# Kernel tuning notes

Hardware: AMD Instinct MI355X
Metric: run time of the kernel (lower is better)

The kernel has to match this reference:

```python
import jax, jax.numpy as jnp
import numpy as np

N = 100000
E = 1000000
IN_C, HID, OUT_C = 64, 64, 40


def setup_inputs() -> dict:
    key = jax.random.key(0)
    ks = jax.random.split(key, 12)
    x = jax.random.normal(ks[0], (N, IN_C), dtype=jnp.float32)
    edge_index = jax.random.randint(ks[1], (2, E), 0, N, dtype=jnp.int64)

    def glorot(k, fan_in, fan_out):
        s = (6.0 / (fan_in + fan_out)) ** 0.5
        return jax.random.uniform(k, (fan_in, fan_out), jnp.float32, -s, s)

    return {
        "x": x,
        "edge_index": edge_index,
        "W1": glorot(ks[2], IN_C, HID), "b1": jnp.zeros((HID,), jnp.float32),
        "W2": glorot(ks[3], HID, HID), "b2": jnp.zeros((HID,), jnp.float32),
        "Wm1": glorot(ks[4], HID, HID), "bm1": jnp.zeros((HID,), jnp.float32),
        "Wm2": glorot(ks[5], HID, OUT_C), "bm2": jnp.zeros((OUT_C,), jnp.float32),
    }


def _gcn_conv(h_in, W, b, src, dst, deg_inv_sqrt):
    # PyG GCNConv: x' = D^{-1/2} (A + I) D^{-1/2} (x W) + b, self-loops added.
    h = h_in @ W                                        # [N, F]
    norm = deg_inv_sqrt[src] * deg_inv_sqrt[dst]        # [E]
    msg = h[src] * norm[:, None]                        # gather + scale
    agg = jax.ops.segment_sum(msg, dst, num_segments=N)  # scatter-add
    # self-loop contribution: deg_i^{-1/2} * deg_i^{-1/2} * h_i
    agg = agg + h * (deg_inv_sqrt * deg_inv_sqrt)[:, None]
    return agg + b


def reference(x, edge_index, W1, b1, W2, b2, Wm1, bm1, Wm2, bm2):
    src, dst = edge_index[0], edge_index[1]
    deg = jax.ops.segment_sum(jnp.ones((E,), jnp.float32), dst, num_segments=N) + 1.0
    deg_inv_sqrt = jax.lax.rsqrt(deg)

    h = _gcn_conv(x, W1, b1, src, dst, deg_inv_sqrt)
    h = jax.nn.relu(h)
    h = _gcn_conv(h, W2, b2, src, dst, deg_inv_sqrt)  # no relu after last conv

    h = jax.nn.relu(h @ Wm1 + bm1)
    out = h @ Wm2 + bm2
    return out
```

## Files before the change

### kernel.cpp

```cpp
#include <hip/hip_runtime.h>
#include <hip/hip_bf16.h>
#include <hip/hip_fp16.h>


namespace {

constexpr int N_NODES = 100000;
constexpr int N_EDGES = 1000000;
constexpr int NBUCK = (N_NODES + 511) / 512;
constexpr int CAP = 8192;
constexpr int EPB_A = 2048;

__global__ __launch_bounds__(256) void zero_detect_kernel(int* bucketCnt, int* flag,
                                                          const unsigned int* __restrict__ w) {
  int t = threadIdx.x;
  if (t < NBUCK) bucketCnt[t] = 0;
  if (t == 0) *flag = 0;
  __syncthreads();
  unsigned any = 0;
  for (int s = 0; s < 8; s++) {
    long long pos = ((long long)(t * 8 + s) * 104729LL) % N_EDGES;
    any |= w[2 * pos + 1];
  }
  if (any) atomicOr(flag, 1);
}

__global__ __launch_bounds__(256) void bucket_kernel(const void* __restrict__ ei,
                                                     const int* __restrict__ flag,
                                                     int* __restrict__ bucketCnt,
                                                     unsigned* __restrict__ tmp) {
  __shared__ int hist[NBUCK];
  __shared__ int basePB[NBUCK];
  __shared__ int cur[NBUCK];
  int t = threadIdx.x;
  if (t < NBUCK) { hist[t] = 0; cur[t] = 0; }
  __syncthreads();

  int e0 = blockIdx.x * EPB_A;
  int is32 = *flag;
  unsigned wreg[8];
  int breg[8];
#pragma unroll
  for (int k = 0; k < 8; k++) {
    int e = e0 + k * 256 + t;
    breg[k] = -1;
    if (e < N_EDGES) {
      int s, d;
      if (is32) {
        const int* p = (const int*)ei;
        s = p[e]; d = p[N_EDGES + e];
      } else {
        const long long* p = (const long long*)ei;
        s = (int)p[e]; d = (int)p[N_EDGES + e];
      }
      wreg[k] = ((unsigned)s << 9) | (unsigned)(d & 511);
      breg[k] = d >> 9;
      atomicAdd(&hist[breg[k]], 1);
    }
  }
  __syncthreads();
  if (t < NBUCK) basePB[t] = hist[t] ? atomicAdd(&bucketCnt[t], hist[t]) : 0;
  __syncthreads();
#pragma unroll
  for (int k = 0; k < 8; k++) {
    if (breg[k] >= 0) {
      int r = atomicAdd(&cur[breg[k]], 1);
      tmp[(size_t)breg[k] * CAP + basePB[breg[k]] + r] = wreg[k];
    }
  }
}

__global__ __launch_bounds__(512) void csr_kernel(const unsigned* __restrict__ tmp,
                                                  const int* __restrict__ bucketCnt,
                                                  int* __restrict__ col,
                                                  int* __restrict__ row_start,
                                                  int* __restrict__ row_end,
                                                  float* __restrict__ dinv) {
  __shared__ int sc[512];
  __shared__ int hist[512];
  __shared__ unsigned stage[CAP];
  int b = blockIdx.x, t = threadIdx.x;
  int myCnt = bucketCnt[b];
  int base = b * CAP;

  hist[t] = 0;
  __syncthreads();
  for (int i = t; i < myCnt; i += 512) {
    unsigned w = tmp[(size_t)base + i];
    stage[i] = w;
    atomicAdd(&hist[w & 511u], 1);
  }
  __syncthreads();

  int deg = hist[t];
  int pdeg = (deg + 7) & ~7;
  sc[t] = pdeg;
  __syncthreads();
#pragma unroll
  for (int off = 1; off < 512; off <<= 1) {
    int u = (t >= off) ? sc[t - off] : 0;
    __syncthreads();
    sc[t] += u;
    __syncthreads();
  }
  int pexcl = sc[t] - pdeg;
  int d = b * 512 + t;
  if (d < N_NODES) {
    row_start[d] = base + pexcl;
    row_end[d] = base + pexcl + pdeg;
    dinv[d] = rsqrtf((float)deg + 1.0f);
  }
  __syncthreads();
  hist[t] = pexcl;
  __syncthreads();
  for (int i = t; i < myCnt; i += 512) {
    unsigned w = stage[i];
    int pos = atomicAdd(&hist[w & 511u], 1);
    col[base + pos] = (int)(w >> 9);
  }
  for (int j = deg; j < pdeg; j++) col[base + pexcl + j] = N_NODES;
}

__device__ inline uint4 pack_half8(const float* v) {
  __half2 h0 = __floats2half2_rn(v[0], v[1]);
  __half2 h1 = __floats2half2_rn(v[2], v[3]);
  __half2 h2 = __floats2half2_rn(v[4], v[5]);
  __half2 h3 = __floats2half2_rn(v[6], v[7]);
  uint4 u;
  u.x = *(unsigned*)&h0; u.y = *(unsigned*)&h1;
  u.z = *(unsigned*)&h2; u.w = *(unsigned*)&h3;
  return u;
}

__global__ __launch_bounds__(256) void gemm_g_kernel(const float* __restrict__ A,
                                                     const float* __restrict__ W,
                                                     const float* __restrict__ dinv,
                                                     __half* __restrict__ g,
                                                     int reluIn) {
  __shared__ float Ws[64 * 64];
  int t = threadIdx.x;
  if (blockIdx.x == 0 && t < 32) ((float*)(g + (size_t)N_NODES * 64))[t] = 0.f;
  for (int i = t; i < 64 * 64 / 4; i += 256) ((float4*)Ws)[i] = ((const float4*)W)[i];
  __syncthreads();

  int rg = t >> 3, cg = t & 7;
  int r0 = blockIdx.x * 128 + rg * 4;
  int c0 = cg * 8;

  float acc[4][8];
#pragma unroll
  for (int i = 0; i < 4; i++)
#pragma unroll
    for (int j = 0; j < 8; j++) acc[i][j] = 0.f;

  const float4* A4 = (const float4*)A;
  for (int kk = 0; kk < 16; kk++) {
    float4 a[4];
#pragma unroll
    for (int i = 0; i < 4; i++) {
      int r = r0 + i;
      float4 v = (r < N_NODES) ? A4[(size_t)r * 16 + kk] : make_float4(0.f, 0.f, 0.f, 0.f);
      if (reluIn) {
        v.x = fmaxf(v.x, 0.f); v.y = fmaxf(v.y, 0.f);
        v.z = fmaxf(v.z, 0.f); v.w = fmaxf(v.w, 0.f);
      }
      a[i] = v;
    }
#pragma unroll
    for (int q = 0; q < 4; q++) {
      int k = kk * 4 + q;
      float w[8];
#pragma unroll
      for (int j = 0; j < 2; j++) *(float4*)&w[4 * j] = *(const float4*)&Ws[k * 64 + c0 + 4 * j];
#pragma unroll
      for (int i = 0; i < 4; i++) {
        float av = q == 0 ? a[i].x : q == 1 ? a[i].y : q == 2 ? a[i].z : a[i].w;
#pragma unroll
        for (int j = 0; j < 8; j++) acc[i][j] = fmaf(av, w[j], acc[i][j]);
      }
    }
  }
#pragma unroll
  for (int i = 0; i < 4; i++) {
    int r = r0 + i;
    if (r < N_NODES) {
      float s = dinv[r];
#pragma unroll
      for (int j = 0; j < 8; j++) acc[i][j] *= s;
      *(uint4*)(g + (size_t)r * 64 + c0) = pack_half8(acc[i]);
    }
  }
}

__global__ __launch_bounds__(256) void aggregate_kernel(const __half* __restrict__ g,
                                                        const int* __restrict__ col,
                                                        const int* __restrict__ row_start,
                                                        const int* __restrict__ row_end,
                                                        const float* __restrict__ dinv,
                                                        const float* __restrict__ bias,
                                                        float* __restrict__ out) {
  int d = blockIdx.x * 4 + (threadIdx.x >> 6);
  int lane = threadIdx.x & 63;
  if (d >= N_NODES) return;
  int e0 = row_start[d], e1 = row_end[d];
  float acc0 = __half2float(g[(size_t)d * 64 + lane]);
  float acc1 = 0.f, acc2 = 0.f, acc3 = 0.f;
  float acc4 = 0.f, acc5 = 0.f, acc6 = 0.f, acc7 = 0.f;
  for (int e = e0; e < e1; e += 8) {
    int4 ca = *(const int4*)(col + e);
    int4 cb = *(const int4*)(col + e + 4);
    float h0 = __half2float(g[(size_t)ca.x * 64 + lane]);
    float h1 = __half2float(g[(size_t)ca.y * 64 + lane]);
    float h2 = __half2float(g[(size_t)ca.z * 64 + lane]);
    float h3 = __half2float(g[(size_t)ca.w * 64 + lane]);
    float h4 = __half2float(g[(size_t)cb.x * 64 + lane]);
    float h5 = __half2float(g[(size_t)cb.y * 64 + lane]);
    float h6 = __half2float(g[(size_t)cb.z * 64 + lane]);
    float h7 = __half2float(g[(size_t)cb.w * 64 + lane]);
    acc0 += h0; acc1 += h1; acc2 += h2; acc3 += h3;
    acc4 += h4; acc5 += h5; acc6 += h6; acc7 += h7;
  }
  float r = ((acc0 + acc1) + (acc2 + acc3)) + ((acc4 + acc5) + (acc6 + acc7));
  out[(size_t)d * 64 + lane] = fmaf(r, dinv[d], bias[lane]);
}

template <int F>
__global__ __launch_bounds__(256) void gemm_kernel(const float* __restrict__ A, const float* __restrict__ W,
                                                   const float* __restrict__ bias, float* __restrict__ C,
                                                   int n, int reluIn, int reluOut) {
  constexpr int CPT = F / 8;
  __shared__ float Ws[64 * F];
  int t = threadIdx.x;
  for (int i = t; i < 64 * F / 4; i += 256) ((float4*)Ws)[i] = ((const float4*)W)[i];
  __syncthreads();

  int rg = t >> 3, cg = t & 7;
  int r0 = blockIdx.x * 128 + rg * 4;
  int c0 = cg * CPT;

  float acc[4][CPT];
#pragma unroll
  for (int i = 0; i < 4; i++)
#pragma unroll
    for (int j = 0; j < CPT; j++) acc[i][j] = 0.f;

  const float4* A4 = (const float4*)A;
  for (int kk = 0; kk < 16; kk++) {
    float4 a[4];
#pragma unroll
    for (int i = 0; i < 4; i++) {
      int r = r0 + i;
      float4 v = (r < n) ? A4[(size_t)r * 16 + kk] : make_float4(0.f, 0.f, 0.f, 0.f);
      if (reluIn) {
        v.x = fmaxf(v.x, 0.f); v.y = fmaxf(v.y, 0.f);
        v.z = fmaxf(v.z, 0.f); v.w = fmaxf(v.w, 0.f);
      }
      a[i] = v;
    }
#pragma unroll
    for (int q = 0; q < 4; q++) {
      int k = kk * 4 + q;
      float w[CPT];
      if constexpr (CPT % 4 == 0) {
#pragma unroll
        for (int j = 0; j < CPT / 4; j++)
          *(float4*)&w[4 * j] = *(const float4*)&Ws[k * F + c0 + 4 * j];
      } else {
#pragma unroll
        for (int j = 0; j < CPT; j++) w[j] = Ws[k * F + c0 + j];
      }
#pragma unroll
      for (int i = 0; i < 4; i++) {
        float av = q == 0 ? a[i].x : q == 1 ? a[i].y : q == 2 ? a[i].z : a[i].w;
#pragma unroll
        for (int j = 0; j < CPT; j++) acc[i][j] = fmaf(av, w[j], acc[i][j]);
      }
    }
  }

  float bv[CPT];
#pragma unroll
  for (int j = 0; j < CPT; j++) bv[j] = bias ? bias[c0 + j] : 0.f;
#pragma unroll
  for (int i = 0; i < 4; i++) {
    int r = r0 + i;
    if (r < n) {
      float* crow = C + (size_t)r * F + c0;
#pragma unroll
      for (int j = 0; j < CPT; j++) {
        float v = acc[i][j] + bv[j];
        if (reluOut) v = fmaxf(v, 0.f);
        crow[j] = v;
      }
    }
  }
}

}

extern "C" void kernel_launch(void* const* d_in, const int* in_sizes, int n_in,
                              void* d_out, int out_size, void* d_ws, size_t ws_size,
                              hipStream_t stream) {
  const float* x   = (const float*)d_in[0];
  const void*  ei  = d_in[1];
  const float* W1  = (const float*)d_in[2];
  const float* b1  = (const float*)d_in[3];
  const float* W2  = (const float*)d_in[4];
  const float* b2  = (const float*)d_in[5];
  const float* Wm1 = (const float*)d_in[6];
  const float* bm1 = (const float*)d_in[7];
  const float* Wm2 = (const float*)d_in[8];
  const float* bm2 = (const float*)d_in[9];
  float* out = (float*)d_out;

  char* ws = (char*)d_ws;
  size_t off = 0;
  auto alloc = [&](size_t bytes) -> void* {
    void* p = ws + off;
    off = (off + bytes + 511) & ~(size_t)511;
    return p;
  };
  int*      flag      = (int*)     alloc(4);
  int*      bucketCnt = (int*)     alloc((size_t)NBUCK * 4);
  unsigned* tmp       = (unsigned*)alloc((size_t)NBUCK * CAP * 4);
  int*      colA      = (int*)     alloc((size_t)NBUCK * CAP * 4);
  int*      rowS      = (int*)     alloc((size_t)N_NODES * 4);
  int*      rowE      = (int*)     alloc((size_t)N_NODES * 4);
  float*    dinv      = (float*)   alloc((size_t)N_NODES * 4);
  __half*   g1        = (__half*)  alloc((size_t)(N_NODES + 1) * 64 * 2);
  float*    hA        = (float*)   alloc((size_t)N_NODES * 64 * 4);
  float*    hB        = (float*)   alloc((size_t)N_NODES * 64 * 4);
  (void)ws_size; (void)in_sizes; (void)n_in; (void)out_size;

  dim3 b256(256);
  int gGemm = (N_NODES + 127) / 128;
  int gAgg  = (N_NODES + 3) / 4;
  int gBkt  = (N_EDGES + EPB_A - 1) / EPB_A;

  zero_detect_kernel<<<1, b256, 0, stream>>>(bucketCnt, flag, (const unsigned int*)ei);
  bucket_kernel<<<gBkt, b256, 0, stream>>>(ei, flag, bucketCnt, tmp);
  csr_kernel<<<NBUCK, dim3(512), 0, stream>>>(tmp, bucketCnt, colA, rowS, rowE, dinv);

  gemm_g_kernel<<<gGemm, b256, 0, stream>>>(x, W1, dinv, g1, 0);
  aggregate_kernel<<<gAgg, b256, 0, stream>>>(g1, colA, rowS, rowE, dinv, b1, hB);

  gemm_g_kernel<<<gGemm, b256, 0, stream>>>(hB, W2, dinv, g1, 1);
  aggregate_kernel<<<gAgg, b256, 0, stream>>>(g1, colA, rowS, rowE, dinv, b2, hB);

  gemm_kernel<64><<<gGemm, b256, 0, stream>>>(hB, Wm1, bm1, hA, N_NODES, 0, 1);
  gemm_kernel<40><<<gGemm, b256, 0, stream>>>(hA, Wm2, bm2, out, N_NODES, 0, 0);
}
```

Before: 279.0 us.

## Fuse the two MLP GEMMs into one kernel and halve aggregate lanes per node

The two final dense layers become a single kernel. The ReLU hidden tile stays in shared memory instead of going through a global intermediate buffer, which removes one 25.6MB write and read and one launch. The aggregation kernel now gives each node half a wave with half2 loads, so eight nodes are processed per block and the gather loads are wider. The fused MLP uses more shared memory per block, which can lower occupancy. The aggregation drops its bounds check and relies on N being divisible by 8.

```diff
diff --git a/kernel.cpp b/kernel.cpp
--- a/kernel.cpp
+++ b/kernel.cpp
@@ -10,6 +10,7 @@
 constexpr int NBUCK = (N_NODES + 511) / 512;
 constexpr int CAP = 8192;
 constexpr int EPB_A = 2048;
+constexpr int TS = 68;
 
 __global__ __launch_bounds__(256) void zero_detect_kernel(int* bucketCnt, int* flag,
                                                           const unsigned int* __restrict__ w) {
@@ -199,99 +200,132 @@
                                                         const float* __restrict__ dinv,
                                                         const float* __restrict__ bias,
                                                         float* __restrict__ out) {
-  int d = blockIdx.x * 4 + (threadIdx.x >> 6);
+  int wave = threadIdx.x >> 6;
   int lane = threadIdx.x & 63;
-  if (d >= N_NODES) return;
-  int e0 = row_start[d], e1 = row_end[d];
-  float acc0 = __half2float(g[(size_t)d * 64 + lane]);
-  float acc1 = 0.f, acc2 = 0.f, acc3 = 0.f;
-  float acc4 = 0.f, acc5 = 0.f, acc6 = 0.f, acc7 = 0.f;
-  for (int e = e0; e < e1; e += 8) {
-    int4 ca = *(const int4*)(col + e);
-    int4 cb = *(const int4*)(col + e + 4);
-    float h0 = __half2float(g[(size_t)ca.x * 64 + lane]);
-    float h1 = __half2float(g[(size_t)ca.y * 64 + lane]);
-    float h2 = __half2float(g[(size_t)ca.z * 64 + lane]);
-    float h3 = __half2float(g[(size_t)ca.w * 64 + lane]);
-    float h4 = __half2float(g[(size_t)cb.x * 64 + lane]);
-    float h5 = __half2float(g[(size_t)cb.y * 64 + lane]);
-    float h6 = __half2float(g[(size_t)cb.z * 64 + lane]);
-    float h7 = __half2float(g[(size_t)cb.w * 64 + lane]);
-    acc0 += h0; acc1 += h1; acc2 += h2; acc3 += h3;
-    acc4 += h4; acc5 += h5; acc6 += h6; acc7 += h7;
-  }
-  float r = ((acc0 + acc1) + (acc2 + acc3)) + ((acc4 + acc5) + (acc6 + acc7));
-  out[(size_t)d * 64 + lane] = fmaf(r, dinv[d], bias[lane]);
-}
-
-template <int F>
-__global__ __launch_bounds__(256) void gemm_kernel(const float* __restrict__ A, const float* __restrict__ W,
-                                                   const float* __restrict__ bias, float* __restrict__ C,
-                                                   int n, int reluIn, int reluOut) {
-  constexpr int CPT = F / 8;
-  __shared__ float Ws[64 * F];
+  int half = lane >> 5;
+  int sub = lane & 31;
+  int d = blockIdx.x * 8 + wave * 2 + half;
+
+  const __half2* g2 = (const __half2*)g;
+  int e0 = row_start[d];
+  int len = row_end[d] - e0;
+
+  float2 a0 = __half22float2(g2[(size_t)d * 32 + sub]);
+  float2 a1 = {0.f, 0.f}, a2 = {0.f, 0.f}, a3 = {0.f, 0.f};
+  float2 a4 = {0.f, 0.f}, a5 = {0.f, 0.f}, a6 = {0.f, 0.f}, a7 = {0.f, 0.f};
+
+  for (int i = 0; i < len; i += 8) {
+    int4 ca = *(const int4*)(col + e0 + i);
+    int4 cb = *(const int4*)(col + e0 + i + 4);
+    float2 h0 = __half22float2(g2[(size_t)ca.x * 32 + sub]);
+    float2 h1 = __half22float2(g2[(size_t)ca.y * 32 + sub]);
+    float2 h2 = __half22float2(g2[(size_t)ca.z * 32 + sub]);
+    float2 h3 = __half22float2(g2[(size_t)ca.w * 32 + sub]);
+    float2 h4 = __half22float2(g2[(size_t)cb.x * 32 + sub]);
+    float2 h5 = __half22float2(g2[(size_t)cb.y * 32 + sub]);
+    float2 h6 = __half22float2(g2[(size_t)cb.z * 32 + sub]);
+    float2 h7 = __half22float2(g2[(size_t)cb.w * 32 + sub]);
+    a0.x += h0.x; a0.y += h0.y; a1.x += h1.x; a1.y += h1.y;
+    a2.x += h2.x; a2.y += h2.y; a3.x += h3.x; a3.y += h3.y;
+    a4.x += h4.x; a4.y += h4.y; a5.x += h5.x; a5.y += h5.y;
+    a6.x += h6.x; a6.y += h6.y; a7.x += h7.x; a7.y += h7.y;
+  }
+  float rx = ((a0.x + a1.x) + (a2.x + a3.x)) + ((a4.x + a5.x) + (a6.x + a7.x));
+  float ry = ((a0.y + a1.y) + (a2.y + a3.y)) + ((a4.y + a5.y) + (a6.y + a7.y));
+  float dv = dinv[d];
+  float2 bv = ((const float2*)bias)[sub];
+  float2 o;
+  o.x = fmaf(rx, dv, bv.x);
+  o.y = fmaf(ry, dv, bv.y);
+  ((float2*)out)[(size_t)d * 32 + sub] = o;
+}
+
+__global__ __launch_bounds__(256) void mlp_kernel(const float* __restrict__ A,
+                                                  const float* __restrict__ Wm1,
+                                                  const float* __restrict__ bm1,
+                                                  const float* __restrict__ Wm2,
+                                                  const float* __restrict__ bm2,
+                                                  float* __restrict__ out) {
+  __shared__ float W1s[64 * 64];
+  __shared__ float W2s[64 * 40];
+  __shared__ float tile[64 * TS];
   int t = threadIdx.x;
-  for (int i = t; i < 64 * F / 4; i += 256) ((float4*)Ws)[i] = ((const float4*)W)[i];
+  for (int i = t; i < 64 * 64 / 4; i += 256) ((float4*)W1s)[i] = ((const float4*)Wm1)[i];
+  for (int i = t; i < 64 * 40 / 4; i += 256) ((float4*)W2s)[i] = ((const float4*)Wm2)[i];
   __syncthreads();
 
   int rg = t >> 3, cg = t & 7;
-  int r0 = blockIdx.x * 128 + rg * 4;
-  int c0 = cg * CPT;
-
-  float acc[4][CPT];
-#pragma unroll
-  for (int i = 0; i < 4; i++)
-#pragma unroll
-    for (int j = 0; j < CPT; j++) acc[i][j] = 0.f;
-
+  int r0 = blockIdx.x * 64 + rg * 2;
+  int c0 = cg * 8;
+
+  float acc[2][8];
+#pragma unroll
+  for (int i = 0; i < 2; i++)
+#pragma unroll
+    for (int j = 0; j < 8; j++) acc[i][j] = bm1[c0 + j];
   const float4* A4 = (const float4*)A;
   for (int kk = 0; kk < 16; kk++) {
-    float4 a[4];
-#pragma unroll
-    for (int i = 0; i < 4; i++) {
+    float4 a[2];
+#pragma unroll
+    for (int i = 0; i < 2; i++) {
       int r = r0 + i;
-      float4 v = (r < n) ? A4[(size_t)r * 16 + kk] : make_float4(0.f, 0.f, 0.f, 0.f);
-      if (reluIn) {
-        v.x = fmaxf(v.x, 0.f); v.y = fmaxf(v.y, 0.f);
-        v.z = fmaxf(v.z, 0.f); v.w = fmaxf(v.w, 0.f);
-      }
-      a[i] = v;
+      a[i] = (r < N_NODES) ? A4[(size_t)r * 16 + kk] : make_float4(0.f, 0.f, 0.f, 0.f);
     }
 #pragma unroll
     for (int q = 0; q < 4; q++) {
       int k = kk * 4 + q;
-      float w[CPT];
-      if constexpr (CPT % 4 == 0) {
-#pragma unroll
-        for (int j = 0; j < CPT / 4; j++)
-          *(float4*)&w[4 * j] = *(const float4*)&Ws[k * F + c0 + 4 * j];
-      } else {
-#pragma unroll
-        for (int j = 0; j < CPT; j++) w[j] = Ws[k * F + c0 + j];
-      }
-#pragma unroll
-      for (int i = 0; i < 4; i++) {
+      float wv[8];
+#pragma unroll
+      for (int j = 0; j < 2; j++) *(float4*)&wv[4 * j] = *(const float4*)&W1s[k * 64 + c0 + 4 * j];
+#pragma unroll
+      for (int i = 0; i < 2; i++) {
         float av = q == 0 ? a[i].x : q == 1 ? a[i].y : q == 2 ? a[i].z : a[i].w;
 #pragma unroll
-        for (int j = 0; j < CPT; j++) acc[i][j] = fmaf(av, w[j], acc[i][j]);
-      }
-    }
-  }
-
-  float bv[CPT];
-#pragma unroll
-  for (int j = 0; j < CPT; j++) bv[j] = bias ? bias[c0 + j] : 0.f;
-#pragma unroll
-  for (int i = 0; i < 4; i++) {
+        for (int j = 0; j < 8; j++) acc[i][j] = fmaf(av, wv[j], acc[i][j]);
+      }
+    }
+  }
+#pragma unroll
+  for (int i = 0; i < 2; i++)
+#pragma unroll
+    for (int j = 0; j < 2; j++) {
+      float4 v;
+      v.x = fmaxf(acc[i][4 * j + 0], 0.f); v.y = fmaxf(acc[i][4 * j + 1], 0.f);
+      v.z = fmaxf(acc[i][4 * j + 2], 0.f); v.w = fmaxf(acc[i][4 * j + 3], 0.f);
+      *(float4*)&tile[(rg * 2 + i) * TS + c0 + 4 * j] = v;
+    }
+  __syncthreads();
+
+  int c5 = cg * 5;
+  float acc2[2][5];
+#pragma unroll
+  for (int i = 0; i < 2; i++)
+#pragma unroll
+    for (int j = 0; j < 5; j++) acc2[i][j] = bm2[c5 + j];
+  for (int kk = 0; kk < 16; kk++) {
+    float4 a[2];
+#pragma unroll
+    for (int i = 0; i < 2; i++) a[i] = *(const float4*)&tile[(rg * 2 + i) * TS + kk * 4];
+#pragma unroll
+    for (int q = 0; q < 4; q++) {
+      int k = kk * 4 + q;
+      float wv[5];
+#pragma unroll
+      for (int j = 0; j < 5; j++) wv[j] = W2s[k * 40 + c5 + j];
+#pragma unroll
+      for (int i = 0; i < 2; i++) {
+        float av = q == 0 ? a[i].x : q == 1 ? a[i].y : q == 2 ? a[i].z : a[i].w;
+#pragma unroll
+        for (int j = 0; j < 5; j++) acc2[i][j] = fmaf(av, wv[j], acc2[i][j]);
+      }
+    }
+  }
+#pragma unroll
+  for (int i = 0; i < 2; i++) {
     int r = r0 + i;
-    if (r < n) {
-      float* crow = C + (size_t)r * F + c0;
-#pragma unroll
-      for (int j = 0; j < CPT; j++) {
-        float v = acc[i][j] + bv[j];
-        if (reluOut) v = fmaxf(v, 0.f);
-        crow[j] = v;
-      }
+    if (r < N_NODES) {
+#pragma unroll
+      for (int j = 0; j < 5; j++) out[(size_t)r * 40 + c5 + j] = acc2[i][j];
     }
   }
 }
@@ -328,13 +362,13 @@
   int*      rowE      = (int*)     alloc((size_t)N_NODES * 4);
   float*    dinv      = (float*)   alloc((size_t)N_NODES * 4);
   __half*   g1        = (__half*)  alloc((size_t)(N_NODES + 1) * 64 * 2);
-  float*    hA        = (float*)   alloc((size_t)N_NODES * 64 * 4);
   float*    hB        = (float*)   alloc((size_t)N_NODES * 64 * 4);
   (void)ws_size; (void)in_sizes; (void)n_in; (void)out_size;
 
   dim3 b256(256);
   int gGemm = (N_NODES + 127) / 128;
-  int gAgg  = (N_NODES + 3) / 4;
+  int gAgg  = N_NODES / 8;
+  int gMlp  = (N_NODES + 63) / 64;
   int gBkt  = (N_EDGES + EPB_A - 1) / EPB_A;
 
   zero_detect_kernel<<<1, b256, 0, stream>>>(bucketCnt, flag, (const unsigned int*)ei);
@@ -347,6 +381,5 @@
   gemm_g_kernel<<<gGemm, b256, 0, stream>>>(hB, W2, dinv, g1, 1);
   aggregate_kernel<<<gAgg, b256, 0, stream>>>(g1, colA, rowS, rowE, dinv, b2, hB);
 
-  gemm_kernel<64><<<gGemm, b256, 0, stream>>>(hB, Wm1, bm1, hA, N_NODES, 0, 1);
-  gemm_kernel<40><<<gGemm, b256, 0, stream>>>(hA, Wm2, bm2, out, N_NODES, 0, 0);
-}
+  mlp_kernel<<<gMlp, b256, 0, stream>>>(hB, Wm1, bm1, Wm2, bm2, out);
+}
```

After: 448.6 us. 1.61x slower.
